# Kernel optimization log

Measured on AMD Instinct MI355X. Metric: run time of the kernel, lower is better.

## Reference

```python
import jax, jax.numpy as jnp
import numpy as np

# Module config (init_kwargs)
K_PERIODS = 5
PMAX = 512
MIN_PERIOD_THRESHOLD = 2

B, T, N = 32, 2048, 128


def setup_inputs() -> dict:
    key = jax.random.key(0)
    x = jax.random.normal(key, (B, T, N), dtype=jnp.float32)
    return {"x": x}


def reference(x):
    """Faithful dense/padded JAX version of PeriodicityTransform.forward (mask=None).

    The torch module emits ragged PeriodGroups keyed by (cycles, period).
    Since jit requires static shapes, we return the same per-(series, freq)
    information in padded form:
      tiles   : [BN, K, T]  flattened folded tile (row-major cycle x period),
                 zero-padded past take = cycles*periods
      periods : [BN, K] int32
      cycles  : [BN, K] int32
    tiles[bn,k,:take].reshape(cycles, period) equals the torch tile exactly.
    """
    Bq, Tq, Nq = x.shape
    BN = Bq * Nq
    seqs = jnp.transpose(x, (0, 2, 1)).reshape(BN, Tq)  # [BN, T]

    # --- _topk_freq ---
    spec = jnp.fft.rfft(seqs, axis=-1)                   # [BN, T//2+1]
    mag2 = spec.real ** 2 + spec.imag ** 2
    mag2 = mag2.at[..., 0].set(0.0)                      # kill DC
    k = min(K_PERIODS, mag2.shape[-1] - 1)
    _, kidx = jax.lax.top_k(mag2, k)                     # [BN, K]
    kidx = jnp.maximum(kidx, 1).astype(jnp.int32)

    # --- period / cycle computation (valid_lengths == T, no mask) ---
    lengths = jnp.int32(Tq)
    periods = lengths // kidx                            # [BN, K]
    periods = jnp.minimum(periods, PMAX)
    min_period = min(MIN_PERIOD_THRESHOLD, Tq)
    periods = jnp.maximum(periods, min_period)
    periods = jnp.maximum(periods, 1)
    cycles = jnp.maximum(lengths // periods, 1)          # [BN, K]

    take = cycles * periods                              # [BN, K], <= T
    t = jnp.arange(Tq, dtype=jnp.int32)                  # [T]
    start = Tq - take                                    # [BN, K]
    gather_idx = jnp.clip(start[..., None] + t, 0, Tq - 1)  # [BN, K, T]
    valid = t[None, None, :] < take[..., None]           # [BN, K, T]

    src = jnp.broadcast_to(seqs[:, None, :], (BN, k, Tq))
    tiles = jnp.take_along_axis(src, gather_idx, axis=-1)
    tiles = jnp.where(valid, tiles, jnp.zeros((), dtype=tiles.dtype))
    return tiles, periods, cycles
```

## Files before the change

### kernel.cpp

```cpp
#include <hip/hip_runtime.h>

#define B_ 32
#define T_ 2048
#define N_ 128
#define K_ 5
#define BN_ (B_ * N_)
#define PMAX_ 512
#define MINP_ 2

static constexpr double PI_D = 3.14159265358979323846264338327950288;
static constexpr float  S2_F = 0.70710678118654752440f;

typedef float vf4 __attribute__((ext_vector_type(4)));

struct cf { float r, i; };

__device__ __forceinline__ void bf_w(cf& u, cf& v, float wr, float wi) {
    const float tr = v.r * wr - v.i * wi;
    const float ti = v.r * wi + v.i * wr;
    v.r = u.r - tr; v.i = u.i - ti;
    u.r += tr;      u.i += ti;
}
__device__ __forceinline__ void bf_1(cf& u, cf& v) {
    const float tr = v.r, ti = v.i;
    v.r = u.r - tr; v.i = u.i - ti;
    u.r += tr;      u.i += ti;
}
__device__ __forceinline__ void bf_mi(cf& u, cf& v) {
    const float tr = v.i, ti = -v.r;
    v.r = u.r - tr; v.i = u.i - ti;
    u.r += tr;      u.i += ti;
}
__device__ __forceinline__ int sw(int i) { return i ^ ((i >> 5) & 31); }

__global__ __launch_bounds__(256) void pt_twiddle(float2* __restrict__ tw) {
    const int m = blockIdx.x * 256 + threadIdx.x;
    if (m < 1024) {
        double s, c;
        sincos(-2.0 * PI_D * (double)m / 2048.0, &s, &c);
        tw[m] = make_float2((float)c, (float)s);
    }
}

__global__ __launch_bounds__(256, 7) void pt_fft_tiles(const float* __restrict__ x,
                                                       float* __restrict__ out,
                                                       const float2* __restrict__ tw) {
    __shared__ __align__(16) float re[2052];
    __shared__ __align__(16) float im[2052];
    __shared__ int sh_take[2][K_];

    const int i0  = blockIdx.x;
    const int q   = ((i0 & 7) << 8) | (i0 >> 3);
    const int bn0 = q * 2;
    const int b   = bn0 >> 7;
    const int n   = bn0 & 127;
    const int tid = threadIdx.x;

    const float* xp = x + (size_t)b * T_ * N_ + n;
    float2 v[8];
#pragma unroll
    for (int m = 0; m < 8; ++m)
        v[m] = *(const float2*)(xp + (size_t)(tid + 256 * m) * N_);
#pragma unroll
    for (int m = 0; m < 8; ++m) {
        const int t = tid + 256 * m;
        const int p = sw((int)(__brev((unsigned)t) >> 21));
        re[p] = v[m].x;
        im[p] = v[m].y;
    }
    __syncthreads();

    {
        const int base = tid * 8;
        cf E[8];
#pragma unroll
        for (int j = 0; j < 8; ++j) { const int p = sw(base + j); E[j].r = re[p]; E[j].i = im[p]; }
        bf_1(E[0], E[1]); bf_1(E[2], E[3]); bf_1(E[4], E[5]); bf_1(E[6], E[7]);
        bf_1(E[0], E[2]); bf_mi(E[1], E[3]); bf_1(E[4], E[6]); bf_mi(E[5], E[7]);
        bf_1(E[0], E[4]); bf_w(E[1], E[5], S2_F, -S2_F);
        bf_mi(E[2], E[6]); bf_w(E[3], E[7], -S2_F, -S2_F);
#pragma unroll
        for (int j = 0; j < 8; ++j) { const int p = sw(base + j); re[p] = E[j].r; im[p] = E[j].i; }
    }
    __syncthreads();

#pragma unroll
    for (int r = 0; r < 2; ++r) {
        const int s    = 4 + 3 * r;
        const int h    = 1 << (s - 1);
        const int bq   = tid & (h - 1);
        const int g    = tid >> (s - 1);
        const int base = g * 8 * h + bq;
        const float2 w1  = tw[bq << (11 - s)];
        const float2 w2a = tw[bq << (10 - s)];
        const float2 w2b = tw[(bq + h) << (10 - s)];
        const float2 w30 = tw[bq << (9 - s)];
        const float2 w31 = tw[(bq + h) << (9 - s)];
        const float2 w32 = tw[(bq + 2 * h) << (9 - s)];
        const float2 w33 = tw[(bq + 3 * h) << (9 - s)];
        cf E[8];
#pragma unroll
        for (int j = 0; j < 8; ++j) { const int p = sw(base + j * h); E[j].r = re[p]; E[j].i = im[p]; }
        bf_w(E[0], E[1], w1.x, w1.y);   bf_w(E[2], E[3], w1.x, w1.y);
        bf_w(E[4], E[5], w1.x, w1.y);   bf_w(E[6], E[7], w1.x, w1.y);
        bf_w(E[0], E[2], w2a.x, w2a.y); bf_w(E[1], E[3], w2b.x, w2b.y);
        bf_w(E[4], E[6], w2a.x, w2a.y); bf_w(E[5], E[7], w2b.x, w2b.y);
        bf_w(E[0], E[4], w30.x, w30.y); bf_w(E[1], E[5], w31.x, w31.y);
        bf_w(E[2], E[6], w32.x, w32.y); bf_w(E[3], E[7], w33.x, w33.y);
#pragma unroll
        for (int j = 0; j < 8; ++j) { const int p = sw(base + j * h); re[p] = E[j].r; im[p] = E[j].i; }
        __syncthreads();
    }

#pragma unroll
    for (int u = 0; u < 2; ++u) {
        const int bb = tid + 256 * u;
        const float2 wA = tw[bb << 1];
        const float2 wB = tw[bb];
        const float2 wC = tw[bb + 512];
        const int p0 = sw(bb), p1 = sw(bb + 512), p2 = sw(bb + 1024), p3 = sw(bb + 1536);
        cf E0 = {re[p0], im[p0]}, E1 = {re[p1], im[p1]};
        cf E2 = {re[p2], im[p2]}, E3 = {re[p3], im[p3]};
        bf_w(E0, E1, wA.x, wA.y); bf_w(E2, E3, wA.x, wA.y);
        bf_w(E0, E2, wB.x, wB.y); bf_w(E1, E3, wC.x, wC.y);
        re[p0] = E0.r; im[p0] = E0.i; re[p1] = E1.r; im[p1] = E1.i;
        re[p2] = E2.r; im[p2] = E2.i; re[p3] = E3.r; im[p3] = E3.i;
    }
    __syncthreads();

    float magsA[4], magsB[4];
#pragma unroll
    for (int m = 0; m < 4; ++m) {
        const int k  = 1 + tid + 256 * m;
        const int nk = 2048 - k;
        const int pk = sw(k), pn = sw(nk);
        const float zr = re[pk], zi = im[pk];
        const float yr = re[pn], yi = im[pn];
        const float ar = zr + yr, ai = zi - yi;
        const float br = zi + yi, bi = yr - zr;
        magsA[m] = ar * ar + ai * ai;
        magsB[m] = br * br + bi * bi;
    }
    __syncthreads();
#pragma unroll
    for (int m = 0; m < 4; ++m) {
        const int pk = sw(1 + tid + 256 * m);
        re[pk] = magsA[m];
        im[pk] = magsB[m];
    }
    __syncthreads();

    const int wid  = tid >> 6;
    const int lane = tid & 63;
    if (wid < 2) {
        const float* marr = wid ? im : re;
        float mv[16];
#pragma unroll
        for (int j = 0; j < 16; ++j) mv[j] = marr[sw(1 + lane + 64 * j)];
        for (int it = 0; it < K_; ++it) {
            float bestv = -2.0f;
            int   besti = 1 << 30;
#pragma unroll
            for (int j = 0; j < 16; ++j) {
                const int k = 1 + lane + 64 * j;
                if (mv[j] > bestv || (mv[j] == bestv && k < besti)) { bestv = mv[j]; besti = k; }
            }
#pragma unroll
            for (int off = 32; off > 0; off >>= 1) {
                const float v3 = __shfl_down(bestv, off);
                const int   i3 = __shfl_down(besti, off);
                if (v3 > bestv || (v3 == bestv && i3 < besti)) { bestv = v3; besti = i3; }
            }
            const int win = __shfl(besti, 0);
#pragma unroll
            for (int j = 0; j < 16; ++j)
                if (1 + lane + 64 * j == win) mv[j] = -1.0f;
            if (lane == 0) {
                int period = T_ / win;
                if (period > PMAX_) period = PMAX_;
                if (period < MINP_) period = MINP_;
                const int cyc = T_ / period;
                sh_take[wid][it] = (period << 16) | (period * cyc);
            }
        }
    }
    __syncthreads();

    const size_t TILES = (size_t)BN_ * K_ * T_;
    if (tid < 2 * K_) {
        const int s2 = tid / K_, k2 = tid % K_;
        const int pk   = sh_take[s2][k2];
        const int per  = pk >> 16;
        const int take = pk & 0xFFFF;
        out[TILES + (size_t)(bn0 + s2) * K_ + k2]                      = (float)per;
        out[TILES + (size_t)BN_ * K_ + (size_t)(bn0 + s2) * K_ + k2]   = (float)(take / per);
    }

#pragma unroll
    for (int m = 0; m < 8; ++m) {
        const int t = tid + 256 * m;
        re[t] = v[m].x;
        im[t] = v[m].y;
    }
    __syncthreads();

    float* rowA = out + (size_t)bn0 * (K_ * T_);
#pragma unroll
    for (int m = 0; m < 20; ++m) {
        const int e  = tid + 256 * m;
        const int s2 = (e >= K_ * (T_ / 4)) ? 1 : 0;
        const int w  = e - s2 * (K_ * (T_ / 4));
        const int k  = w >> 9;
        const int p4 = (w & 511) << 2;
        const int take  = sh_take[s2][k] & 0xFFFF;
        const int start = T_ - take;
        const vf4* sq4 = (const vf4*)(s2 ? im : re);
        const int idx = start + p4;
        int a0 = idx >> 2;
        if (a0 > 511) a0 = 511;
        const int sh = idx & 3;
        const vf4 lo = sq4[a0];
        const vf4 hi = sq4[a0 + 1];
        float r0, r1, r2, r3;
        if (sh == 0)      { r0 = lo.x; r1 = lo.y; r2 = lo.z; r3 = lo.w; }
        else if (sh == 1) { r0 = lo.y; r1 = lo.z; r2 = lo.w; r3 = hi.x; }
        else if (sh == 2) { r0 = lo.z; r1 = lo.w; r2 = hi.x; r3 = hi.y; }
        else              { r0 = lo.w; r1 = hi.x; r2 = hi.y; r3 = hi.z; }
        vf4 vv;
        vv.x = (p4 + 0 < take) ? r0 : 0.0f;
        vv.y = (p4 + 1 < take) ? r1 : 0.0f;
        vv.z = (p4 + 2 < take) ? r2 : 0.0f;
        vv.w = (p4 + 3 < take) ? r3 : 0.0f;
        *(vf4*)(rowA + (size_t)(s2 * K_ + k) * T_ + p4) = vv;
    }
}

extern "C" void kernel_launch(void* const* d_in, const int* in_sizes, int n_in,
                              void* d_out, int out_size, void* d_ws, size_t ws_size,
                              hipStream_t stream) {
    const float* x = (const float*)d_in[0];
    float* out = (float*)d_out;
    float2* tw = (float2*)d_ws;

    pt_twiddle<<<dim3(4), dim3(256), 0, stream>>>(tw);
    pt_fft_tiles<<<dim3(BN_ / 2), dim3(256), 0, stream>>>(x, out, tw);
}
```

Baseline: 216.6 us.

## Switch to one-series-per-block real FFT via half-length complex FFT

Each block previously computed one 2048-point complex FFT that carried two real series (one in the real part, one in the imaginary part). It now handles a single series by packing its even and odd samples into a 1024-point complex FFT of radix-4 stages, then recovering the real spectrum with a twiddle post-processing step. The grid doubles to one block per series, shared memory per block shrinks, launch bounds rise to 8 and only one wave runs the top-k. This trades per-block FFT work and parallelism against strided scalar global loads (two loads per float2 instead of one) and more radix-4 stages, each with its own barrier.

```diff
diff --git a/kernel.cpp b/kernel.cpp
--- a/kernel.cpp
+++ b/kernel.cpp
@@ -9,7 +9,6 @@
 #define MINP_ 2
 
 static constexpr double PI_D = 3.14159265358979323846264338327950288;
-static constexpr float  S2_F = 0.70710678118654752440f;
 
 typedef float vf4 __attribute__((ext_vector_type(4)));
 
@@ -42,121 +41,93 @@
     }
 }
 
-__global__ __launch_bounds__(256, 7) void pt_fft_tiles(const float* __restrict__ x,
+__global__ __launch_bounds__(256, 8) void pt_fft_tiles(const float* __restrict__ x,
                                                        float* __restrict__ out,
                                                        const float2* __restrict__ tw) {
-    __shared__ __align__(16) float re[2052];
-    __shared__ __align__(16) float im[2052];
-    __shared__ int sh_take[2][K_];
+    __shared__ __align__(16) float L[2056];
+    __shared__ float M[1028];
+    __shared__ int sh_take[K_];
 
     const int i0  = blockIdx.x;
-    const int q   = ((i0 & 7) << 8) | (i0 >> 3);
-    const int bn0 = q * 2;
-    const int b   = bn0 >> 7;
-    const int n   = bn0 & 127;
+    const int bn  = ((i0 & 7) << 9) | (i0 >> 3);
+    const int b   = bn >> 7;
+    const int n   = bn & 127;
     const int tid = threadIdx.x;
 
     const float* xp = x + (size_t)b * T_ * N_ + n;
-    float2 v[8];
-#pragma unroll
-    for (int m = 0; m < 8; ++m)
-        v[m] = *(const float2*)(xp + (size_t)(tid + 256 * m) * N_);
-#pragma unroll
-    for (int m = 0; m < 8; ++m) {
-        const int t = tid + 256 * m;
-        const int p = sw((int)(__brev((unsigned)t) >> 21));
-        re[p] = v[m].x;
-        im[p] = v[m].y;
+    float2 sv[4];
+#pragma unroll
+    for (int m = 0; m < 4; ++m) {
+        const int mm = tid + 256 * m;
+        sv[m].x = xp[(size_t)(2 * mm) * N_];
+        sv[m].y = xp[(size_t)(2 * mm + 1) * N_];
+        const int p = sw((int)(__brev((unsigned)mm) >> 22));
+        L[p]        = sv[m].x;
+        L[1028 + p] = sv[m].y;
     }
     __syncthreads();
 
     {
-        const int base = tid * 8;
-        cf E[8];
-#pragma unroll
-        for (int j = 0; j < 8; ++j) { const int p = sw(base + j); E[j].r = re[p]; E[j].i = im[p]; }
-        bf_1(E[0], E[1]); bf_1(E[2], E[3]); bf_1(E[4], E[5]); bf_1(E[6], E[7]);
-        bf_1(E[0], E[2]); bf_mi(E[1], E[3]); bf_1(E[4], E[6]); bf_mi(E[5], E[7]);
-        bf_1(E[0], E[4]); bf_w(E[1], E[5], S2_F, -S2_F);
-        bf_mi(E[2], E[6]); bf_w(E[3], E[7], -S2_F, -S2_F);
-#pragma unroll
-        for (int j = 0; j < 8; ++j) { const int p = sw(base + j); re[p] = E[j].r; im[p] = E[j].i; }
-    }
-    __syncthreads();
-
-#pragma unroll
-    for (int r = 0; r < 2; ++r) {
-        const int s    = 4 + 3 * r;
-        const int h    = 1 << (s - 1);
+        const int base = tid * 4;
+        cf E[4];
+#pragma unroll
+        for (int j = 0; j < 4; ++j) { const int p = sw(base + j); E[j].r = L[p]; E[j].i = L[1028 + p]; }
+        bf_1(E[0], E[1]); bf_1(E[2], E[3]);
+        bf_1(E[0], E[2]); bf_mi(E[1], E[3]);
+#pragma unroll
+        for (int j = 0; j < 4; ++j) { const int p = sw(base + j); L[p] = E[j].r; L[1028 + p] = E[j].i; }
+    }
+    __syncthreads();
+
+#pragma unroll
+    for (int r = 1; r < 5; ++r) {
+        const int h    = 1 << (2 * r);
         const int bq   = tid & (h - 1);
-        const int g    = tid >> (s - 1);
-        const int base = g * 8 * h + bq;
-        const float2 w1  = tw[bq << (11 - s)];
-        const float2 w2a = tw[bq << (10 - s)];
-        const float2 w2b = tw[(bq + h) << (10 - s)];
-        const float2 w30 = tw[bq << (9 - s)];
-        const float2 w31 = tw[(bq + h) << (9 - s)];
-        const float2 w32 = tw[(bq + 2 * h) << (9 - s)];
-        const float2 w33 = tw[(bq + 3 * h) << (9 - s)];
-        cf E[8];
-#pragma unroll
-        for (int j = 0; j < 8; ++j) { const int p = sw(base + j * h); E[j].r = re[p]; E[j].i = im[p]; }
+        const int g    = tid >> (2 * r);
+        const int base = g * 4 * h + bq;
+        const float2 w1  = tw[bq << (10 - 2 * r)];
+        const float2 w2a = tw[bq << (9 - 2 * r)];
+        const float2 w2b = tw[(bq + h) << (9 - 2 * r)];
+        cf E[4];
+#pragma unroll
+        for (int j = 0; j < 4; ++j) { const int p = sw(base + j * h); E[j].r = L[p]; E[j].i = L[1028 + p]; }
         bf_w(E[0], E[1], w1.x, w1.y);   bf_w(E[2], E[3], w1.x, w1.y);
-        bf_w(E[4], E[5], w1.x, w1.y);   bf_w(E[6], E[7], w1.x, w1.y);
         bf_w(E[0], E[2], w2a.x, w2a.y); bf_w(E[1], E[3], w2b.x, w2b.y);
-        bf_w(E[4], E[6], w2a.x, w2a.y); bf_w(E[5], E[7], w2b.x, w2b.y);
-        bf_w(E[0], E[4], w30.x, w30.y); bf_w(E[1], E[5], w31.x, w31.y);
-        bf_w(E[2], E[6], w32.x, w32.y); bf_w(E[3], E[7], w33.x, w33.y);
-#pragma unroll
-        for (int j = 0; j < 8; ++j) { const int p = sw(base + j * h); re[p] = E[j].r; im[p] = E[j].i; }
+#pragma unroll
+        for (int j = 0; j < 4; ++j) { const int p = sw(base + j * h); L[p] = E[j].r; L[1028 + p] = E[j].i; }
         __syncthreads();
     }
 
 #pragma unroll
-    for (int u = 0; u < 2; ++u) {
-        const int bb = tid + 256 * u;
-        const float2 wA = tw[bb << 1];
-        const float2 wB = tw[bb];
-        const float2 wC = tw[bb + 512];
-        const int p0 = sw(bb), p1 = sw(bb + 512), p2 = sw(bb + 1024), p3 = sw(bb + 1536);
-        cf E0 = {re[p0], im[p0]}, E1 = {re[p1], im[p1]};
-        cf E2 = {re[p2], im[p2]}, E3 = {re[p3], im[p3]};
-        bf_w(E0, E1, wA.x, wA.y); bf_w(E2, E3, wA.x, wA.y);
-        bf_w(E0, E2, wB.x, wB.y); bf_w(E1, E3, wC.x, wC.y);
-        re[p0] = E0.r; im[p0] = E0.i; re[p1] = E1.r; im[p1] = E1.i;
-        re[p2] = E2.r; im[p2] = E2.i; re[p3] = E3.r; im[p3] = E3.i;
-    }
-    __syncthreads();
-
-    float magsA[4], magsB[4];
-#pragma unroll
     for (int m = 0; m < 4; ++m) {
-        const int k  = 1 + tid + 256 * m;
-        const int nk = 2048 - k;
-        const int pk = sw(k), pn = sw(nk);
-        const float zr = re[pk], zi = im[pk];
-        const float yr = re[pn], yi = im[pn];
-        const float ar = zr + yr, ai = zi - yi;
-        const float br = zi + yi, bi = yr - zr;
-        magsA[m] = ar * ar + ai * ai;
-        magsB[m] = br * br + bi * bi;
-    }
-    __syncthreads();
-#pragma unroll
-    for (int m = 0; m < 4; ++m) {
-        const int pk = sw(1 + tid + 256 * m);
-        re[pk] = magsA[m];
-        im[pk] = magsB[m];
+        const int k = 1 + tid + 256 * m;
+        float mg;
+        if (k == 1024) {
+            const int p0 = sw(0);
+            const float d = L[p0] - L[1028 + p0];
+            mg = 4.0f * d * d;
+        } else {
+            const int pk = sw(k), pn = sw(1024 - k);
+            const float zr = L[pk],  zi = L[1028 + pk];
+            const float yr = L[pn],  yi = L[1028 + pn];
+            const float Ar = zr + yr, Ai = zi - yi;
+            const float Br = zr - yr, Bi = zi + yi;
+            const float2 w = tw[k];
+            const float Cr = w.x * Bi + w.y * Br;
+            const float Ci = w.y * Bi - w.x * Br;
+            const float sr = Ar + Cr, si = Ai + Ci;
+            mg = sr * sr + si * si;
+        }
+        M[sw(k - 1)] = mg;
     }
     __syncthreads();
 
     const int wid  = tid >> 6;
     const int lane = tid & 63;
-    if (wid < 2) {
-        const float* marr = wid ? im : re;
+    if (wid == 0) {
         float mv[16];
 #pragma unroll
-        for (int j = 0; j < 16; ++j) mv[j] = marr[sw(1 + lane + 64 * j)];
+        for (int j = 0; j < 16; ++j) mv[j] = M[sw(lane + 64 * j)];
         for (int it = 0; it < K_; ++it) {
             float bestv = -2.0f;
             int   besti = 1 << 30;
@@ -180,47 +151,42 @@
                 if (period > PMAX_) period = PMAX_;
                 if (period < MINP_) period = MINP_;
                 const int cyc = T_ / period;
-                sh_take[wid][it] = (period << 16) | (period * cyc);
+                sh_take[it] = (period << 16) | (period * cyc);
             }
         }
     }
+
+#pragma unroll
+    for (int m = 0; m < 4; ++m) {
+        const int mm = tid + 256 * m;
+        *(float2*)(L + 2 * mm) = sv[m];
+    }
     __syncthreads();
 
     const size_t TILES = (size_t)BN_ * K_ * T_;
-    if (tid < 2 * K_) {
-        const int s2 = tid / K_, k2 = tid % K_;
-        const int pk   = sh_take[s2][k2];
+    if (tid < K_) {
+        const int pk   = sh_take[tid];
         const int per  = pk >> 16;
         const int take = pk & 0xFFFF;
-        out[TILES + (size_t)(bn0 + s2) * K_ + k2]                      = (float)per;
-        out[TILES + (size_t)BN_ * K_ + (size_t)(bn0 + s2) * K_ + k2]   = (float)(take / per);
-    }
-
-#pragma unroll
-    for (int m = 0; m < 8; ++m) {
-        const int t = tid + 256 * m;
-        re[t] = v[m].x;
-        im[t] = v[m].y;
-    }
-    __syncthreads();
-
-    float* rowA = out + (size_t)bn0 * (K_ * T_);
-#pragma unroll
-    for (int m = 0; m < 20; ++m) {
+        out[TILES + (size_t)bn * K_ + tid]                      = (float)per;
+        out[TILES + (size_t)BN_ * K_ + (size_t)bn * K_ + tid]   = (float)(take / per);
+    }
+
+    float* row = out + (size_t)bn * (K_ * T_);
+    const vf4* L4 = (const vf4*)L;
+#pragma unroll
+    for (int m = 0; m < 10; ++m) {
         const int e  = tid + 256 * m;
-        const int s2 = (e >= K_ * (T_ / 4)) ? 1 : 0;
-        const int w  = e - s2 * (K_ * (T_ / 4));
-        const int k  = w >> 9;
-        const int p4 = (w & 511) << 2;
-        const int take  = sh_take[s2][k] & 0xFFFF;
+        const int k  = e >> 9;
+        const int p4 = (e & 511) << 2;
+        const int take  = sh_take[k] & 0xFFFF;
         const int start = T_ - take;
-        const vf4* sq4 = (const vf4*)(s2 ? im : re);
         const int idx = start + p4;
         int a0 = idx >> 2;
         if (a0 > 511) a0 = 511;
         const int sh = idx & 3;
-        const vf4 lo = sq4[a0];
-        const vf4 hi = sq4[a0 + 1];
+        const vf4 lo = L4[a0];
+        const vf4 hi = L4[a0 + 1];
         float r0, r1, r2, r3;
         if (sh == 0)      { r0 = lo.x; r1 = lo.y; r2 = lo.z; r3 = lo.w; }
         else if (sh == 1) { r0 = lo.y; r1 = lo.z; r2 = lo.w; r3 = hi.x; }
@@ -231,7 +197,7 @@
         vv.y = (p4 + 1 < take) ? r1 : 0.0f;
         vv.z = (p4 + 2 < take) ? r2 : 0.0f;
         vv.w = (p4 + 3 < take) ? r3 : 0.0f;
-        *(vf4*)(rowA + (size_t)(s2 * K_ + k) * T_ + p4) = vv;
+        *(vf4*)(row + (size_t)k * T_ + p4) = vv;
     }
 }
 
@@ -243,5 +209,5 @@
     float2* tw = (float2*)d_ws;
 
     pt_twiddle<<<dim3(4), dim3(256), 0, stream>>>(tw);
-    pt_fft_tiles<<<dim3(BN_ / 2), dim3(256), 0, stream>>>(x, out, tw);
-}
+    pt_fft_tiles<<<dim3(BN_), dim3(256), 0, stream>>>(x, out, tw);
+}
```

Result: slower. 224.5 us (+3.6%).

## Process four series per block with 16-byte loads and separate tile staging buffers

Applied to the files above, without the earlier changes.

Each block now loads four adjacent series with 16-byte vector loads and runs the two-series FFT/top-k/tile pipeline twice. The raw sequences are staged in separate shared buffers (sqA/sqB), and __syncthreads is replaced by a custom LDS-wait-plus-barrier helper with scheduling fences. The aim is wider global reads and lower barrier overhead. In exchange, shared memory per block doubles, the launch-bounds occupancy hint drops from 7 to 4, and there are half as many blocks, so less parallelism and more serialized work per block.

```diff
diff --git a/kernel.cpp b/kernel.cpp
--- a/kernel.cpp
+++ b/kernel.cpp
@@ -33,6 +33,14 @@
 }
 __device__ __forceinline__ int sw(int i) { return i ^ ((i >> 5) & 31); }
 
+__device__ __forceinline__ void bar_lgkm() {
+    __builtin_amdgcn_sched_barrier(0);
+    asm volatile("s_waitcnt lgkmcnt(0)" ::: "memory");
+    __builtin_amdgcn_s_barrier();
+    asm volatile("" ::: "memory");
+    __builtin_amdgcn_sched_barrier(0);
+}
+
 __global__ __launch_bounds__(256) void pt_twiddle(float2* __restrict__ tw) {
     const int m = blockIdx.x * 256 + threadIdx.x;
     if (m < 1024) {
@@ -42,196 +50,205 @@
     }
 }
 
-__global__ __launch_bounds__(256, 7) void pt_fft_tiles(const float* __restrict__ x,
+__global__ __launch_bounds__(256, 4) void pt_fft_tiles(const float* __restrict__ x,
                                                        float* __restrict__ out,
                                                        const float2* __restrict__ tw) {
     __shared__ __align__(16) float re[2052];
     __shared__ __align__(16) float im[2052];
+    __shared__ __align__(16) float sqA[2052];
+    __shared__ __align__(16) float sqB[2052];
     __shared__ int sh_take[2][K_];
 
     const int i0  = blockIdx.x;
-    const int q   = ((i0 & 7) << 8) | (i0 >> 3);
-    const int bn0 = q * 2;
-    const int b   = bn0 >> 7;
-    const int n   = bn0 & 127;
+    const int q   = ((i0 & 7) << 7) | (i0 >> 3);
+    const int bnb = q * 4;
+    const int b   = bnb >> 7;
+    const int n   = bnb & 127;
     const int tid = threadIdx.x;
 
     const float* xp = x + (size_t)b * T_ * N_ + n;
-    float2 v[8];
+    vf4 sv[8];
 #pragma unroll
     for (int m = 0; m < 8; ++m)
-        v[m] = *(const float2*)(xp + (size_t)(tid + 256 * m) * N_);
-#pragma unroll
-    for (int m = 0; m < 8; ++m) {
-        const int t = tid + 256 * m;
-        const int p = sw((int)(__brev((unsigned)t) >> 21));
-        re[p] = v[m].x;
-        im[p] = v[m].y;
-    }
-    __syncthreads();
-
-    {
-        const int base = tid * 8;
-        cf E[8];
-#pragma unroll
-        for (int j = 0; j < 8; ++j) { const int p = sw(base + j); E[j].r = re[p]; E[j].i = im[p]; }
-        bf_1(E[0], E[1]); bf_1(E[2], E[3]); bf_1(E[4], E[5]); bf_1(E[6], E[7]);
-        bf_1(E[0], E[2]); bf_mi(E[1], E[3]); bf_1(E[4], E[6]); bf_mi(E[5], E[7]);
-        bf_1(E[0], E[4]); bf_w(E[1], E[5], S2_F, -S2_F);
-        bf_mi(E[2], E[6]); bf_w(E[3], E[7], -S2_F, -S2_F);
-#pragma unroll
-        for (int j = 0; j < 8; ++j) { const int p = sw(base + j); re[p] = E[j].r; im[p] = E[j].i; }
-    }
-    __syncthreads();
-
-#pragma unroll
-    for (int r = 0; r < 2; ++r) {
-        const int s    = 4 + 3 * r;
-        const int h    = 1 << (s - 1);
-        const int bq   = tid & (h - 1);
-        const int g    = tid >> (s - 1);
-        const int base = g * 8 * h + bq;
-        const float2 w1  = tw[bq << (11 - s)];
-        const float2 w2a = tw[bq << (10 - s)];
-        const float2 w2b = tw[(bq + h) << (10 - s)];
-        const float2 w30 = tw[bq << (9 - s)];
-        const float2 w31 = tw[(bq + h) << (9 - s)];
-        const float2 w32 = tw[(bq + 2 * h) << (9 - s)];
-        const float2 w33 = tw[(bq + 3 * h) << (9 - s)];
-        cf E[8];
-#pragma unroll
-        for (int j = 0; j < 8; ++j) { const int p = sw(base + j * h); E[j].r = re[p]; E[j].i = im[p]; }
-        bf_w(E[0], E[1], w1.x, w1.y);   bf_w(E[2], E[3], w1.x, w1.y);
-        bf_w(E[4], E[5], w1.x, w1.y);   bf_w(E[6], E[7], w1.x, w1.y);
-        bf_w(E[0], E[2], w2a.x, w2a.y); bf_w(E[1], E[3], w2b.x, w2b.y);
-        bf_w(E[4], E[6], w2a.x, w2a.y); bf_w(E[5], E[7], w2b.x, w2b.y);
-        bf_w(E[0], E[4], w30.x, w30.y); bf_w(E[1], E[5], w31.x, w31.y);
-        bf_w(E[2], E[6], w32.x, w32.y); bf_w(E[3], E[7], w33.x, w33.y);
-#pragma unroll
-        for (int j = 0; j < 8; ++j) { const int p = sw(base + j * h); re[p] = E[j].r; im[p] = E[j].i; }
-        __syncthreads();
-    }
-
-#pragma unroll
-    for (int u = 0; u < 2; ++u) {
-        const int bb = tid + 256 * u;
-        const float2 wA = tw[bb << 1];
-        const float2 wB = tw[bb];
-        const float2 wC = tw[bb + 512];
-        const int p0 = sw(bb), p1 = sw(bb + 512), p2 = sw(bb + 1024), p3 = sw(bb + 1536);
-        cf E0 = {re[p0], im[p0]}, E1 = {re[p1], im[p1]};
-        cf E2 = {re[p2], im[p2]}, E3 = {re[p3], im[p3]};
-        bf_w(E0, E1, wA.x, wA.y); bf_w(E2, E3, wA.x, wA.y);
-        bf_w(E0, E2, wB.x, wB.y); bf_w(E1, E3, wC.x, wC.y);
-        re[p0] = E0.r; im[p0] = E0.i; re[p1] = E1.r; im[p1] = E1.i;
-        re[p2] = E2.r; im[p2] = E2.i; re[p3] = E3.r; im[p3] = E3.i;
-    }
-    __syncthreads();
-
-    float magsA[4], magsB[4];
-#pragma unroll
-    for (int m = 0; m < 4; ++m) {
-        const int k  = 1 + tid + 256 * m;
-        const int nk = 2048 - k;
-        const int pk = sw(k), pn = sw(nk);
-        const float zr = re[pk], zi = im[pk];
-        const float yr = re[pn], yi = im[pn];
-        const float ar = zr + yr, ai = zi - yi;
-        const float br = zi + yi, bi = yr - zr;
-        magsA[m] = ar * ar + ai * ai;
-        magsB[m] = br * br + bi * bi;
-    }
-    __syncthreads();
-#pragma unroll
-    for (int m = 0; m < 4; ++m) {
-        const int pk = sw(1 + tid + 256 * m);
-        re[pk] = magsA[m];
-        im[pk] = magsB[m];
-    }
-    __syncthreads();
-
-    const int wid  = tid >> 6;
-    const int lane = tid & 63;
-    if (wid < 2) {
-        const float* marr = wid ? im : re;
-        float mv[16];
-#pragma unroll
-        for (int j = 0; j < 16; ++j) mv[j] = marr[sw(1 + lane + 64 * j)];
-        for (int it = 0; it < K_; ++it) {
-            float bestv = -2.0f;
-            int   besti = 1 << 30;
-#pragma unroll
-            for (int j = 0; j < 16; ++j) {
-                const int k = 1 + lane + 64 * j;
-                if (mv[j] > bestv || (mv[j] == bestv && k < besti)) { bestv = mv[j]; besti = k; }
+        sv[m] = *(const vf4*)(xp + (size_t)(tid + 256 * m) * N_);
+
+    const size_t TILES = (size_t)BN_ * K_ * T_;
+
+#pragma unroll
+    for (int P = 0; P < 2; ++P) {
+        const int bn0 = bnb + 2 * P;
+
+#pragma unroll
+        for (int m = 0; m < 8; ++m) {
+            const int t = tid + 256 * m;
+            const int p = sw((int)(__brev((unsigned)t) >> 21));
+            re[p] = P ? sv[m].z : sv[m].x;
+            im[p] = P ? sv[m].w : sv[m].y;
+        }
+        bar_lgkm();
+
+        {
+            const int base = tid * 8;
+            cf E[8];
+#pragma unroll
+            for (int j = 0; j < 8; ++j) { const int p = sw(base + j); E[j].r = re[p]; E[j].i = im[p]; }
+            bf_1(E[0], E[1]); bf_1(E[2], E[3]); bf_1(E[4], E[5]); bf_1(E[6], E[7]);
+            bf_1(E[0], E[2]); bf_mi(E[1], E[3]); bf_1(E[4], E[6]); bf_mi(E[5], E[7]);
+            bf_1(E[0], E[4]); bf_w(E[1], E[5], S2_F, -S2_F);
+            bf_mi(E[2], E[6]); bf_w(E[3], E[7], -S2_F, -S2_F);
+#pragma unroll
+            for (int j = 0; j < 8; ++j) { const int p = sw(base + j); re[p] = E[j].r; im[p] = E[j].i; }
+        }
+        bar_lgkm();
+
+#pragma unroll
+        for (int r = 0; r < 2; ++r) {
+            const int s    = 4 + 3 * r;
+            const int h    = 1 << (s - 1);
+            const int bq   = tid & (h - 1);
+            const int g    = tid >> (s - 1);
+            const int base = g * 8 * h + bq;
+            const float2 w1  = tw[bq << (11 - s)];
+            const float2 w2a = tw[bq << (10 - s)];
+            const float2 w2b = tw[(bq + h) << (10 - s)];
+            const float2 w30 = tw[bq << (9 - s)];
+            const float2 w31 = tw[(bq + h) << (9 - s)];
+            const float2 w32 = tw[(bq + 2 * h) << (9 - s)];
+            const float2 w33 = tw[(bq + 3 * h) << (9 - s)];
+            cf E[8];
+#pragma unroll
+            for (int j = 0; j < 8; ++j) { const int p = sw(base + j * h); E[j].r = re[p]; E[j].i = im[p]; }
+            bf_w(E[0], E[1], w1.x, w1.y);   bf_w(E[2], E[3], w1.x, w1.y);
+            bf_w(E[4], E[5], w1.x, w1.y);   bf_w(E[6], E[7], w1.x, w1.y);
+            bf_w(E[0], E[2], w2a.x, w2a.y); bf_w(E[1], E[3], w2b.x, w2b.y);
+            bf_w(E[4], E[6], w2a.x, w2a.y); bf_w(E[5], E[7], w2b.x, w2b.y);
+            bf_w(E[0], E[4], w30.x, w30.y); bf_w(E[1], E[5], w31.x, w31.y);
+            bf_w(E[2], E[6], w32.x, w32.y); bf_w(E[3], E[7], w33.x, w33.y);
+#pragma unroll
+            for (int j = 0; j < 8; ++j) { const int p = sw(base + j * h); re[p] = E[j].r; im[p] = E[j].i; }
+            bar_lgkm();
+        }
+
+#pragma unroll
+        for (int u = 0; u < 2; ++u) {
+            const int bb = tid + 256 * u;
+            const float2 wA = tw[bb << 1];
+            const float2 wB = tw[bb];
+            const float2 wC = tw[bb + 512];
+            const int p0 = sw(bb), p1 = sw(bb + 512), p2 = sw(bb + 1024), p3 = sw(bb + 1536);
+            cf E0 = {re[p0], im[p0]}, E1 = {re[p1], im[p1]};
+            cf E2 = {re[p2], im[p2]}, E3 = {re[p3], im[p3]};
+            bf_w(E0, E1, wA.x, wA.y); bf_w(E2, E3, wA.x, wA.y);
+            bf_w(E0, E2, wB.x, wB.y); bf_w(E1, E3, wC.x, wC.y);
+            re[p0] = E0.r; im[p0] = E0.i; re[p1] = E1.r; im[p1] = E1.i;
+            re[p2] = E2.r; im[p2] = E2.i; re[p3] = E3.r; im[p3] = E3.i;
+        }
+        bar_lgkm();
+
+        float magsA[4], magsB[4];
+#pragma unroll
+        for (int m = 0; m < 4; ++m) {
+            const int k  = 1 + tid + 256 * m;
+            const int nk = 2048 - k;
+            const int pk = sw(k), pn = sw(nk);
+            const float zr = re[pk], zi = im[pk];
+            const float yr = re[pn], yi = im[pn];
+            const float ar = zr + yr, ai = zi - yi;
+            const float br = zi + yi, bi = yr - zr;
+            magsA[m] = ar * ar + ai * ai;
+            magsB[m] = br * br + bi * bi;
+        }
+        bar_lgkm();
+#pragma unroll
+        for (int m = 0; m < 4; ++m) {
+            const int pk = sw(1 + tid + 256 * m);
+            re[pk] = magsA[m];
+            im[pk] = magsB[m];
+        }
+        bar_lgkm();
+
+        const int wid  = tid >> 6;
+        const int lane = tid & 63;
+        if (wid < 2) {
+            const float* marr = wid ? im : re;
+            float mv[16];
+#pragma unroll
+            for (int j = 0; j < 16; ++j) mv[j] = marr[sw(1 + lane + 64 * j)];
+            for (int it = 0; it < K_; ++it) {
+                float bestv = -2.0f;
+                int   besti = 1 << 30;
+#pragma unroll
+                for (int j = 0; j < 16; ++j) {
+                    const int k = 1 + lane + 64 * j;
+                    if (mv[j] > bestv || (mv[j] == bestv && k < besti)) { bestv = mv[j]; besti = k; }
+                }
+#pragma unroll
+                for (int off = 32; off > 0; off >>= 1) {
+                    const float v3 = __shfl_down(bestv, off);
+                    const int   i3 = __shfl_down(besti, off);
+                    if (v3 > bestv || (v3 == bestv && i3 < besti)) { bestv = v3; besti = i3; }
+                }
+                const int win = __shfl(besti, 0);
+#pragma unroll
+                for (int j = 0; j < 16; ++j)
+                    if (1 + lane + 64 * j == win) mv[j] = -1.0f;
+                if (lane == 0) {
+                    int period = T_ / win;
+                    if (period > PMAX_) period = PMAX_;
+                    if (period < MINP_) period = MINP_;
+                    const int cyc = T_ / period;
+                    sh_take[wid][it] = (period << 16) | (period * cyc);
+                }
             }
-#pragma unroll
-            for (int off = 32; off > 0; off >>= 1) {
-                const float v3 = __shfl_down(bestv, off);
-                const int   i3 = __shfl_down(besti, off);
-                if (v3 > bestv || (v3 == bestv && i3 < besti)) { bestv = v3; besti = i3; }
-            }
-            const int win = __shfl(besti, 0);
-#pragma unroll
-            for (int j = 0; j < 16; ++j)
-                if (1 + lane + 64 * j == win) mv[j] = -1.0f;
-            if (lane == 0) {
-                int period = T_ / win;
-                if (period > PMAX_) period = PMAX_;
-                if (period < MINP_) period = MINP_;
-                const int cyc = T_ / period;
-                sh_take[wid][it] = (period << 16) | (period * cyc);
-            }
-        }
-    }
-    __syncthreads();
-
-    const size_t TILES = (size_t)BN_ * K_ * T_;
-    if (tid < 2 * K_) {
-        const int s2 = tid / K_, k2 = tid % K_;
-        const int pk   = sh_take[s2][k2];
-        const int per  = pk >> 16;
-        const int take = pk & 0xFFFF;
-        out[TILES + (size_t)(bn0 + s2) * K_ + k2]                      = (float)per;
-        out[TILES + (size_t)BN_ * K_ + (size_t)(bn0 + s2) * K_ + k2]   = (float)(take / per);
-    }
-
-#pragma unroll
-    for (int m = 0; m < 8; ++m) {
-        const int t = tid + 256 * m;
-        re[t] = v[m].x;
-        im[t] = v[m].y;
-    }
-    __syncthreads();
-
-    float* rowA = out + (size_t)bn0 * (K_ * T_);
-#pragma unroll
-    for (int m = 0; m < 20; ++m) {
-        const int e  = tid + 256 * m;
-        const int s2 = (e >= K_ * (T_ / 4)) ? 1 : 0;
-        const int w  = e - s2 * (K_ * (T_ / 4));
-        const int k  = w >> 9;
-        const int p4 = (w & 511) << 2;
-        const int take  = sh_take[s2][k] & 0xFFFF;
-        const int start = T_ - take;
-        const vf4* sq4 = (const vf4*)(s2 ? im : re);
-        const int idx = start + p4;
-        int a0 = idx >> 2;
-        if (a0 > 511) a0 = 511;
-        const int sh = idx & 3;
-        const vf4 lo = sq4[a0];
-        const vf4 hi = sq4[a0 + 1];
-        float r0, r1, r2, r3;
-        if (sh == 0)      { r0 = lo.x; r1 = lo.y; r2 = lo.z; r3 = lo.w; }
-        else if (sh == 1) { r0 = lo.y; r1 = lo.z; r2 = lo.w; r3 = hi.x; }
-        else if (sh == 2) { r0 = lo.z; r1 = lo.w; r2 = hi.x; r3 = hi.y; }
-        else              { r0 = lo.w; r1 = hi.x; r2 = hi.y; r3 = hi.z; }
-        vf4 vv;
-        vv.x = (p4 + 0 < take) ? r0 : 0.0f;
-        vv.y = (p4 + 1 < take) ? r1 : 0.0f;
-        vv.z = (p4 + 2 < take) ? r2 : 0.0f;
-        vv.w = (p4 + 3 < take) ? r3 : 0.0f;
-        *(vf4*)(rowA + (size_t)(s2 * K_ + k) * T_ + p4) = vv;
+        }
+        bar_lgkm();
+
+#pragma unroll
+        for (int m = 0; m < 8; ++m) {
+            const int t = tid + 256 * m;
+            sqA[t] = P ? sv[m].z : sv[m].x;
+            sqB[t] = P ? sv[m].w : sv[m].y;
+        }
+        bar_lgkm();
+
+        if (tid < 2 * K_) {
+            const int s2 = tid / K_, k2 = tid % K_;
+            const int pk   = sh_take[s2][k2];
+            const int per  = pk >> 16;
+            const int take = pk & 0xFFFF;
+            out[TILES + (size_t)(bn0 + s2) * K_ + k2]                      = (float)per;
+            out[TILES + (size_t)BN_ * K_ + (size_t)(bn0 + s2) * K_ + k2]   = (float)(take / per);
+        }
+
+        float* rowA = out + (size_t)bn0 * (K_ * T_);
+#pragma unroll
+        for (int m = 0; m < 20; ++m) {
+            const int e  = tid + 256 * m;
+            const int s2 = (e >= K_ * (T_ / 4)) ? 1 : 0;
+            const int w  = e - s2 * (K_ * (T_ / 4));
+            const int k  = w >> 9;
+            const int p4 = (w & 511) << 2;
+            const int take  = sh_take[s2][k] & 0xFFFF;
+            const int start = T_ - take;
+            const vf4* sq4 = (const vf4*)(s2 ? sqB : sqA);
+            const int idx = start + p4;
+            int a0 = idx >> 2;
+            if (a0 > 511) a0 = 511;
+            const int sh = idx & 3;
+            const vf4 lo = sq4[a0];
+            const vf4 hi = sq4[a0 + 1];
+            float r0, r1, r2, r3;
+            if (sh == 0)      { r0 = lo.x; r1 = lo.y; r2 = lo.z; r3 = lo.w; }
+            else if (sh == 1) { r0 = lo.y; r1 = lo.z; r2 = lo.w; r3 = hi.x; }
+            else if (sh == 2) { r0 = lo.z; r1 = lo.w; r2 = hi.x; r3 = hi.y; }
+            else              { r0 = lo.w; r1 = hi.x; r2 = hi.y; r3 = hi.z; }
+            vf4 vv;
+            vv.x = (p4 + 0 < take) ? r0 : 0.0f;
+            vv.y = (p4 + 1 < take) ? r1 : 0.0f;
+            vv.z = (p4 + 2 < take) ? r2 : 0.0f;
+            vv.w = (p4 + 3 < take) ? r3 : 0.0f;
+            *(vf4*)(rowA + (size_t)(s2 * K_ + k) * T_ + p4) = vv;
+        }
     }
 }
 
@@ -243,5 +260,5 @@
     float2* tw = (float2*)d_ws;
 
     pt_twiddle<<<dim3(4), dim3(256), 0, stream>>>(tw);
-    pt_fft_tiles<<<dim3(BN_ / 2), dim3(256), 0, stream>>>(x, out, tw);
-}
+    pt_fft_tiles<<<dim3(BN_ / 4), dim3(256), 0, stream>>>(x, out, tw);
+}
```

Result: slower. 242.3 us (+11.8%).

## Replace shared-memory FFT stage exchanges with warp shuffles

Applied to the files above, without the earlier changes.

The two radix-8 middle FFT stages now exchange data between lanes through __shfl_xor transposes held in registers, where before each stage round-tripped through LDS with a __syncthreads in between. This drops two LDS write/read passes and two block barriers per FFT. In exchange it adds 48 shuffles per thread plus select logic, and it relies on each 64-lane wavefront covering exactly 512 points.

```diff
diff --git a/kernel.cpp b/kernel.cpp
--- a/kernel.cpp
+++ b/kernel.cpp
@@ -33,6 +33,17 @@
 }
 __device__ __forceinline__ int sw(int i) { return i ^ ((i >> 5) & 31); }
 
+__device__ __forceinline__ void xsw1(float& a, float& b, int tid, int L) {
+    const float snd = (tid & L) ? a : b;
+    const float got = __shfl_xor(snd, L, 64);
+    if (tid & L) a = got; else b = got;
+}
+#define XSTAGE(L, P0a, P0b, P1a, P1b, P2a, P2b, P3a, P3b)                      \
+    xsw1(E[P0a].r, E[P0b].r, tid, (L)); xsw1(E[P0a].i, E[P0b].i, tid, (L));    \
+    xsw1(E[P1a].r, E[P1b].r, tid, (L)); xsw1(E[P1a].i, E[P1b].i, tid, (L));    \
+    xsw1(E[P2a].r, E[P2b].r, tid, (L)); xsw1(E[P2a].i, E[P2b].i, tid, (L));    \
+    xsw1(E[P3a].r, E[P3b].r, tid, (L)); xsw1(E[P3a].i, E[P3b].i, tid, (L));
+
 __global__ __launch_bounds__(256) void pt_twiddle(float2* __restrict__ tw) {
     const int m = blockIdx.x * 256 + threadIdx.x;
     if (m < 1024) {
@@ -70,47 +81,63 @@
     }
     __syncthreads();
 
+    cf E[8];
+
     {
         const int base = tid * 8;
-        cf E[8];
 #pragma unroll
         for (int j = 0; j < 8; ++j) { const int p = sw(base + j); E[j].r = re[p]; E[j].i = im[p]; }
         bf_1(E[0], E[1]); bf_1(E[2], E[3]); bf_1(E[4], E[5]); bf_1(E[6], E[7]);
         bf_1(E[0], E[2]); bf_mi(E[1], E[3]); bf_1(E[4], E[6]); bf_mi(E[5], E[7]);
         bf_1(E[0], E[4]); bf_w(E[1], E[5], S2_F, -S2_F);
         bf_mi(E[2], E[6]); bf_w(E[3], E[7], -S2_F, -S2_F);
-#pragma unroll
-        for (int j = 0; j < 8; ++j) { const int p = sw(base + j); re[p] = E[j].r; im[p] = E[j].i; }
-    }
-    __syncthreads();
-
-#pragma unroll
-    for (int r = 0; r < 2; ++r) {
-        const int s    = 4 + 3 * r;
-        const int h    = 1 << (s - 1);
-        const int bq   = tid & (h - 1);
-        const int g    = tid >> (s - 1);
-        const int base = g * 8 * h + bq;
-        const float2 w1  = tw[bq << (11 - s)];
-        const float2 w2a = tw[bq << (10 - s)];
-        const float2 w2b = tw[(bq + h) << (10 - s)];
-        const float2 w30 = tw[bq << (9 - s)];
-        const float2 w31 = tw[(bq + h) << (9 - s)];
-        const float2 w32 = tw[(bq + 2 * h) << (9 - s)];
-        const float2 w33 = tw[(bq + 3 * h) << (9 - s)];
-        cf E[8];
-#pragma unroll
-        for (int j = 0; j < 8; ++j) { const int p = sw(base + j * h); E[j].r = re[p]; E[j].i = im[p]; }
+    }
+
+    XSTAGE(1, 0,1, 2,3, 4,5, 6,7)
+    XSTAGE(2, 0,2, 1,3, 4,6, 5,7)
+    XSTAGE(4, 0,4, 1,5, 2,6, 3,7)
+
+    {
+        const int bq = tid & 7;
+        const float2 w1  = tw[bq << 7];
+        const float2 w2a = tw[bq << 6];
+        const float2 w2b = tw[(bq + 8) << 6];
+        const float2 w30 = tw[bq << 5];
+        const float2 w31 = tw[(bq + 8) << 5];
+        const float2 w32 = tw[(bq + 16) << 5];
+        const float2 w33 = tw[(bq + 24) << 5];
         bf_w(E[0], E[1], w1.x, w1.y);   bf_w(E[2], E[3], w1.x, w1.y);
         bf_w(E[4], E[5], w1.x, w1.y);   bf_w(E[6], E[7], w1.x, w1.y);
         bf_w(E[0], E[2], w2a.x, w2a.y); bf_w(E[1], E[3], w2b.x, w2b.y);
         bf_w(E[4], E[6], w2a.x, w2a.y); bf_w(E[5], E[7], w2b.x, w2b.y);
         bf_w(E[0], E[4], w30.x, w30.y); bf_w(E[1], E[5], w31.x, w31.y);
         bf_w(E[2], E[6], w32.x, w32.y); bf_w(E[3], E[7], w33.x, w33.y);
-#pragma unroll
-        for (int j = 0; j < 8; ++j) { const int p = sw(base + j * h); re[p] = E[j].r; im[p] = E[j].i; }
-        __syncthreads();
-    }
+    }
+
+    XSTAGE(8,  0,1, 2,3, 4,5, 6,7)
+    XSTAGE(16, 0,2, 1,3, 4,6, 5,7)
+    XSTAGE(32, 0,4, 1,5, 2,6, 3,7)
+
+    {
+        const int bq = tid & 63;
+        const float2 w1  = tw[bq << 4];
+        const float2 w2a = tw[bq << 3];
+        const float2 w2b = tw[(bq + 64) << 3];
+        const float2 w30 = tw[bq << 2];
+        const float2 w31 = tw[(bq + 64) << 2];
+        const float2 w32 = tw[(bq + 128) << 2];
+        const float2 w33 = tw[(bq + 192) << 2];
+        bf_w(E[0], E[1], w1.x, w1.y);   bf_w(E[2], E[3], w1.x, w1.y);
+        bf_w(E[4], E[5], w1.x, w1.y);   bf_w(E[6], E[7], w1.x, w1.y);
+        bf_w(E[0], E[2], w2a.x, w2a.y); bf_w(E[1], E[3], w2b.x, w2b.y);
+        bf_w(E[4], E[6], w2a.x, w2a.y); bf_w(E[5], E[7], w2b.x, w2b.y);
+        bf_w(E[0], E[4], w30.x, w30.y); bf_w(E[1], E[5], w31.x, w31.y);
+        bf_w(E[2], E[6], w32.x, w32.y); bf_w(E[3], E[7], w33.x, w33.y);
+        const int base = (tid >> 6) * 512 + (tid & 63);
+#pragma unroll
+        for (int j = 0; j < 8; ++j) { const int p = sw(base + j * 64); re[p] = E[j].r; im[p] = E[j].i; }
+    }
+    __syncthreads();
 
 #pragma unroll
     for (int u = 0; u < 2; ++u) {
```

Result: no change. 214.8 us (-0.8%).
